# Kernel optimization log

Hardware: AMD Instinct MI355X
Metric: run time of the kernel (lower is better)

## Reference

```python
import jax, jax.numpy as jnp
import numpy as np

WS = (3, 8, 8)          # (t, h, w) window
SHIFT = (0, 4, 4)
HEADS = 6
DIM = 120
HD = DIM // HEADS
SCALE = HD ** -0.5
N = WS[0] * WS[1] * WS[2]   # 192 tokens per window
NQ = N // 3                 # 64 query tokens (last frame)


def _rel_pos_index():
    cd, ch, cw = np.arange(WS[0]), np.arange(WS[1]), np.arange(WS[2])
    c2 = np.stack(np.meshgrid(cd, ch, cw, indexing='ij')).reshape(3, -1)      # (3, N)
    c1 = np.stack(np.meshgrid(np.arange(1), ch, cw, indexing='ij')).reshape(3, -1)  # (3, NQ)
    rel = (c1[:, :, None] - c2[:, None, :]).transpose(1, 2, 0)                # (NQ, N, 3)
    rel = rel + np.array([WS[0] - 1, WS[1] - 1, WS[2] - 1])
    idx = rel[..., 0] * (2 * WS[1] - 1) * (2 * WS[2] - 1) + rel[..., 1] * (2 * WS[2] - 1) + rel[..., 2]
    return idx.astype(np.int32)  # values in [0, 3*15*15)


def _shift_attn_mask(h, w):
    # standard Swin shifted-window mask, tiled over the 3 frames
    img = np.zeros((h, w), np.int32)
    cnt = 0
    for hs in (slice(0, -WS[1]), slice(-WS[1], -SHIFT[1]), slice(-SHIFT[1], None)):
        for ws_ in (slice(0, -WS[2]), slice(-WS[2], -SHIFT[2]), slice(-SHIFT[2], None)):
            img[hs, ws_] = cnt
            cnt += 1
    win = img.reshape(h // WS[1], WS[1], w // WS[2], WS[2]).transpose(0, 2, 1, 3).reshape(-1, WS[1] * WS[2])
    m2 = win[:, None, :] - win[:, :, None]
    m2 = np.where(m2 != 0, -100.0, 0.0).astype(np.float32)  # (nW, 64, 64)
    return np.tile(m2, (1, 3, 3))                            # (nW, 192, 192)


def setup_inputs() -> dict:
    key = jax.random.key(0)
    ks = jax.random.split(key, 10)
    b, t, h, w, c = 1, 3, 256, 256, DIM
    nW = (h // WS[1]) * (w // WS[2])
    B_ = b * nW
    return {
        'x': jax.random.normal(ks[0], (b, t, h, w, c), jnp.float32),
        'quary0': jax.random.normal(ks[1], (B_, NQ, c), jnp.float32),
        'quary1': jax.random.normal(ks[2], (B_, NQ, c), jnp.float32),
        'qkv_w': jax.random.normal(ks[3], (3 * c, c), jnp.float32) * 0.02,
        'qkv_b': jnp.zeros((3 * c,), jnp.float32),
        'proj_w': jax.random.normal(ks[4], (c, c), jnp.float32) * 0.02,
        'proj_b': jnp.zeros((c,), jnp.float32),
        'rpb_table': jax.random.normal(ks[5], (WS[0] * (2 * WS[1] - 1) * (2 * WS[2] - 1), HEADS), jnp.float32) * 0.02,
        'pm_w': jax.random.normal(ks[6], (1, c), jnp.float32) * 0.02,
        'pm_b': jnp.zeros((1,), jnp.float32),
        'attn_mask': jnp.asarray(_shift_attn_mask(h, w)),
        'rel_idx': jnp.asarray(_rel_pos_index()),
    }


def reference(x, quary0, quary1, qkv_w, qkv_b, proj_w, proj_b, rpb_table, pm_w, pm_b, attn_mask, rel_idx):
    b, t, h, w, c = x.shape
    # cyclic shift
    x = jnp.roll(x, (-SHIFT[0], -SHIFT[1], -SHIFT[2]), axis=(1, 2, 3))
    # window partition -> (B_, N, c)
    xw = x.reshape(b, t // WS[0], WS[0], h // WS[1], WS[1], w // WS[2], WS[2], c)
    xw = xw.transpose(0, 1, 3, 5, 2, 4, 6, 7).reshape(-1, N, c)
    B_ = xw.shape[0]
    # adaptive mask prediction (eval path: hard threshold; sigmoid(s/T)>=0.5 <=> s>=0)
    pred_q = jax.lax.stop_gradient(xw[:, 2 * NQ:, :])
    soft = jnp.abs(pred_q - quary0) @ pm_w.T + pm_b          # (B_, NQ, 1)
    pred = (soft >= 0).astype(x.dtype)
    # qkv
    qkv = (xw @ qkv_w.T + qkv_b).reshape(B_, N, 3, HEADS, HD).transpose(2, 0, 3, 1, 4)
    q = qkv[0][:, :, 2 * NQ:, :] * SCALE                      # (B_, H, NQ, hd)
    k, v = qkv[1], qkv[2]                                     # (B_, H, N, hd)
    attn = jnp.einsum('bhqd,bhkd->bhqk', q, k)                # (B_, H, NQ, N)
    # gathered relative position bias
    rpb = rpb_table[rel_idx.reshape(-1)].reshape(NQ, N, HEADS).transpose(2, 0, 1)
    attn = attn + rpb[None]
    # shift mask
    nW = attn_mask.shape[0]
    attn = attn.reshape(b, nW, HEADS, NQ, N) + attn_mask[None, :, None, 2 * NQ:, :]
    attn = jax.nn.softmax(attn.reshape(B_, HEADS, NQ, N), axis=-1)
    out = jnp.einsum('bhqk,bhkd->bqhd', attn, v).reshape(B_, NQ, c)
    # output projection + token-pruning blend (math-equivalent to gather/fill eval path)
    x1 = out @ proj_w.T + proj_b
    x_pred = x1 * pred + quary1 * (1.0 - pred)
    xo = jnp.concatenate([x_pred, pred], axis=-1)             # (B_, NQ, c+1)
    # single-frame window reverse
    xo = xo.reshape(b, h // WS[1], w // WS[2], WS[1], WS[2], c + 1)
    xo = xo.transpose(0, 1, 3, 2, 4, 5).reshape(b, h, w, c + 1)
    xo = jnp.roll(xo, (SHIFT[1], SHIFT[2]), axis=(1, 2))
    return xo
```

## Files before the change

kernel.cpp:

```cpp
#include <hip/hip_runtime.h>
#include <math.h>

#define NT 256

typedef __attribute__((ext_vector_type(8))) short s16x8;
typedef __attribute__((ext_vector_type(4))) float f32x4;

#define KVF_OFF 0
#define QF_OFF  73728
#define PJF_OFF 122880
#define RPB_OFF 172032

__device__ __forceinline__ unsigned short f2bf(float f) {
    union { float f; unsigned int i; } v; v.f = f;
    unsigned int x = v.i;
    x += 0x7fffu + ((x >> 16) & 1u);
    return (unsigned short)(x >> 16);
}
__device__ __forceinline__ unsigned int pk2(float a, float b) {
    return (unsigned int)f2bf(a) | ((unsigned int)f2bf(b) << 16);
}

#define MFMA(a, b, c) __builtin_amdgcn_mfma_f32_16x16x32_bf16(a, b, c, 0, 0, 0)

__global__ void prep(const float* __restrict__ qkv_w,
                     const float* __restrict__ proj_w,
                     const float* __restrict__ rpb_table,
                     const int*   __restrict__ rel_idx,
                     unsigned char* __restrict__ wsb)
{
    int gid = blockIdx.x * blockDim.x + threadIdx.x;
    int nthr = gridDim.x * blockDim.x;
    unsigned short* KVF = (unsigned short*)(wsb + KVF_OFF);
    unsigned short* QF  = (unsigned short*)(wsb + QF_OFF);
    unsigned short* PJF = (unsigned short*)(wsb + PJF_OFF);
    float*          RPB = (float*)(wsb + RPB_OFF);

    for (int f = gid; f < 6 * 3 * 4 * 512; f += nthr) {
        int q = f & 511, rest = f >> 9;
        int kk = rest & 3, rest2 = rest >> 2;
        int nt = rest2 % 3, h = rest2 / 3;
        int ln = q >> 3, j = q & 7;
        int l15 = ln & 15, qd = ln >> 4;
        int nglob = nt * 16 + l15, k = kk * 32 + qd * 8 + j;
        float v = 0.f;
        if (k < 120 && nglob < 40) {
            int row = (nglob < 20) ? (120 + h * 20 + nglob) : (240 + h * 20 + nglob - 20);
            v = qkv_w[row * 120 + k];
        }
        KVF[f] = f2bf(v);
    }
    for (int f = gid; f < 6 * 2 * 4 * 512; f += nthr) {
        int q = f & 511, rest = f >> 9;
        int kk = rest & 3, rest2 = rest >> 2;
        int nt = rest2 & 1, h = rest2 >> 1;
        int ln = q >> 3, j = q & 7;
        int l15 = ln & 15, qd = ln >> 4;
        int nn = nt * 16 + l15, k = kk * 32 + qd * 8 + j;
        int row = h * 20 + nn;
        float v = (k < 120) ? qkv_w[row * 120 + k] : 0.f;
        QF[f] = f2bf(v);
    }
    for (int f = gid; f < 6 * 8 * 512; f += nthr) {
        int q = f & 511, rest = f >> 9;
        int ct = rest & 7, h = rest >> 3;
        int ln = q >> 3, j = q & 7;
        int l15 = ln & 15, qd = ln >> 4;
        int c = ct * 16 + l15, k = qd * 8 + j;
        float v = (k < 20 && c < 120) ? proj_w[c * 120 + h * 20 + k] : 0.f;
        PJF[f] = f2bf(v);
    }
    for (int i = gid; i < 6 * 192 * 64; i += nthr) {
        int r = i & 63, n = (i >> 6) % 192, h = i / (192 * 64);
        RPB[i] = rpb_table[rel_idx[r * 192 + n] * 6 + h];
    }
}

__global__ __launch_bounds__(NT, 2)
void swin_mfma(const float* __restrict__ x,
               const float* __restrict__ quary0,
               const float* __restrict__ quary1,
               const float* __restrict__ qkv_b,
               const float* __restrict__ proj_b,
               const float* __restrict__ pm_w,
               const float* __restrict__ pm_b,
               const unsigned char* __restrict__ wsb,
               float* __restrict__ out)
{
    __shared__ alignas(16) unsigned char smem[77968];
    unsigned short* xw = (unsigned short*)smem;
    unsigned short* ks = (unsigned short*)(smem + 46096);
    unsigned short* qs = (unsigned short*)(smem + 55312);
    unsigned short* vt = (unsigned short*)(smem + 61456);
    float* pred_s = (float*)(smem + 77456);
    int*   grp_s  = (int*)(smem + 77712);

    const int tid = threadIdx.x;
    const int wv = tid >> 6, ln = tid & 63;
    const int l15 = ln & 15, qd = ln >> 4;
    const int widx = blockIdx.x;
    const int wh = widx >> 5, ww = widx & 31;
    const float SCALE = 0.22360679774997896f;

    const unsigned short* KVF = (const unsigned short*)(wsb + KVF_OFF);
    const unsigned short* QF  = (const unsigned short*)(wsb + QF_OFF);
    const unsigned short* PJF = (const unsigned short*)(wsb + PJF_OFF);
    const float*          RPB = (const float*)(wsb + RPB_OFF);

    for (int e = tid; e < 192 * 30; e += NT) {
        int n = e / 30, c4 = e % 30;
        int f = n >> 6, ii = (n >> 3) & 7, jj = n & 7;
        int y0 = (wh * 8 + ii + 4) & 255;
        int x0 = (ww * 8 + jj + 4) & 255;
        float4 val = *(const float4*)(x + (((size_t)(f * 256 + y0)) * 256 + x0) * 120 + c4 * 4);
        unsigned int lo = pk2(val.x, val.y);
        unsigned int hi = pk2(val.z, val.w);
        unsigned int off = (unsigned)(n * 120 + c4 * 4);
        *(unsigned int*)(xw + off)     = lo;
        *(unsigned int*)(xw + off + 2) = hi;
    }
    if (tid < 8) xw[192 * 120 + tid] = 0;
    for (int e = tid; e < 192 * 4; e += NT) ks[(e >> 2) * 24 + 20 + (e & 3)] = 0;
    for (int e = tid; e < 2 * 64 * 4; e += NT)
        qs[(e >> 8) * 1536 + ((e >> 2) & 63) * 24 + 20 + (e & 3)] = 0;
    if (tid < 64) {
        int ii = tid >> 3, jj = tid & 7;
        int y0 = (wh * 8 + ii + 4) & 255;
        int x0 = (ww * 8 + jj + 4) & 255;
        int hg = (y0 >= 248) + (y0 >= 252);
        int wg = (x0 >= 248) + (x0 >= 252);
        grp_s[tid] = hg * 3 + wg;
    }
    {
        int r = tid >> 2, j = tid & 3;
        int ii = r >> 3, jj = r & 7;
        int y0 = (wh * 8 + ii + 4) & 255;
        int x0 = (ww * 8 + jj + 4) & 255;
        const float* xr  = x + (((size_t)(2 * 256 + y0)) * 256 + x0) * 120;
        const float* q0r = quary0 + ((size_t)widx * 64 + r) * 120;
        float acc = 0.f;
        for (int ch = j * 30; ch < j * 30 + 30; ++ch)
            acc += fabsf(xr[ch] - q0r[ch]) * pm_w[ch];
        acc += __shfl_xor(acc, 1);
        acc += __shfl_xor(acc, 2);
        if (j == 0) pred_s[r] = (acc + pm_b[0] >= 0.f) ? 1.f : 0.f;
    }
    __syncthreads();

    auto kvjob = [&](int mt, int nt, int hh, int pty) {
        const unsigned short* arow  = xw + (mt * 16 + l15) * 120;
        const unsigned short* bbase = KVF + ((hh * 3 + nt) * 4) * 512 + ln * 8;
        f32x4 acc = {0.f, 0.f, 0.f, 0.f};
        #pragma unroll
        for (int kk = 0; kk < 4; ++kk)
            acc = MFMA(*(const s16x8*)(arow + kk * 32 + qd * 8),
                       *(const s16x8*)(bbase + kk * 512), acc);
        int nglob = nt * 16 + l15;
        if (nglob < 40) {
            float bias = qkv_b[nglob < 20 ? (120 + hh * 20 + nglob)
                                          : (240 + hh * 20 + nglob - 20)];
            #pragma unroll
            for (int reg = 0; reg < 4; ++reg) {
                int tok = mt * 16 + qd * 4 + reg;
                unsigned short vb = f2bf(acc[reg] + bias);
                if (nglob < 20) ks[tok * 24 + nglob] = vb;
                else            vt[pty * 4000 + (nglob - 20) * 200 + tok] = vb;
            }
        }
    };
    auto qjob = [&](int mt, int nt, int hh, int pty) {
        const unsigned short* arow  = xw + (128 + mt * 16 + l15) * 120;
        const unsigned short* bbase = QF + ((hh * 2 + nt) * 4) * 512 + ln * 8;
        f32x4 acc = {0.f, 0.f, 0.f, 0.f};
        #pragma unroll
        for (int kk = 0; kk < 4; ++kk)
            acc = MFMA(*(const s16x8*)(arow + kk * 32 + qd * 8),
                       *(const s16x8*)(bbase + kk * 512), acc);
        int nn = nt * 16 + l15;
        if (nn < 20) {
            float bias = qkv_b[hh * 20 + nn];
            #pragma unroll
            for (int reg = 0; reg < 4; ++reg)
                qs[pty * 1536 + (mt * 16 + qd * 4 + reg) * 24 + nn] =
                    f2bf((acc[reg] + bias) * SCALE);
        }
    };

    for (int e = wv; e < 44; e += 4) {
        if (e < 36) kvjob(e % 12, e / 12, 0, 0);
        else        { int t = e - 36; qjob(t & 3, t >> 2, 0, 0); }
    }
    __syncthreads();

    const int q_l = wv * 16 + l15;
    const int gq = grp_s[q_l];
    unsigned long long mbits = 0ull;
    #pragma unroll
    for (int t = 0; t < 12; ++t)
        #pragma unroll
        for (int r = 0; r < 4; ++r) {
            int tok = t * 16 + qd * 4 + r;
            if (gq != grp_s[tok & 63]) mbits |= (1ull << (t * 4 + r));
        }
    const int srcA = (((qd * 2) & 3) << 4) | l15;
    const int srcB = (((qd * 2 + 1) & 3) << 4) | l15;
    const int msel = qd >> 1;
    const s16x8 zf = {0, 0, 0, 0, 0, 0, 0, 0};

    f32x4 pacc[8];
    #pragma unroll
    for (int i = 0; i < 8; ++i) { f32x4 z = {0.f,0.f,0.f,0.f}; pacc[i] = z; }

    for (int h = 0; h < 6; ++h) {
        const int pr = h & 1, pw = (h + 1) & 1;

        const float* rbase = RPB + ((size_t)(h * 192 + qd * 4)) * 64 + q_l;
        float vals[48];
        #pragma unroll
        for (int t = 0; t < 12; ++t)
            #pragma unroll
            for (int r = 0; r < 4; ++r)
                vals[t * 4 + r] = rbase[(t * 16 + r) * 64]
                                + (((mbits >> (t * 4 + r)) & 1ull) ? -100.f : 0.f);

        if (h < 5) {
            for (int e = wv; e < 20; e += 4) {
                if (e < 12) kvjob(e, 2, h + 1, pw);
                else        { int t = e - 12; qjob(t & 3, t >> 2, h + 1, pw); }
            }
        }

        s16x8 bQ = zf;
        if (qd < 3) bQ = *(const s16x8*)(qs + pr * 1536 + q_l * 24 + qd * 8);
        f32x4 sc[12];
        #pragma unroll
        for (int t = 0; t < 12; ++t) {
            s16x8 aK = *(const s16x8*)(ks + (t * 16 + l15) * 24 + qd * 8);
            f32x4 z = {0.f, 0.f, 0.f, 0.f};
            sc[t] = MFMA(aK, bQ, z);
        }
        float m = -1e30f;
        #pragma unroll
        for (int t = 0; t < 12; ++t)
            #pragma unroll
            for (int r = 0; r < 4; ++r) {
                float v = vals[t * 4 + r] + sc[t][r];
                vals[t * 4 + r] = v; m = fmaxf(m, v);
            }
        m = fmaxf(m, __shfl_xor(m, 16));
        m = fmaxf(m, __shfl_xor(m, 32));
        __syncthreads();

        if (h < 5) {
            for (int e = wv; e < 24; e += 4)
                kvjob(e % 12, (e < 12) ? 0 : 1, h + 1, pw);
        }

        float s = 0.f;
        #pragma unroll
        for (int i = 0; i < 48; ++i) { float ev = __expf(vals[i] - m); vals[i] = ev; s += ev; }
        s += __shfl_xor(s, 16);
        s += __shfl_xor(s, 32);
        float inv = 1.0f / s;

        unsigned int plo[12], phi[12];
        #pragma unroll
        for (int t = 0; t < 12; ++t) {
            plo[t] = pk2(vals[t * 4 + 0] * inv, vals[t * 4 + 1] * inv);
            phi[t] = pk2(vals[t * 4 + 2] * inv, vals[t * 4 + 3] * inv);
        }

        f32x4 o0 = {0.f,0.f,0.f,0.f}, o1 = {0.f,0.f,0.f,0.f};
        #pragma unroll
        for (int kk = 0; kk < 6; ++kk) {
            unsigned int a0 = __shfl(plo[2 * kk],     srcA);
            unsigned int a1 = __shfl(plo[2 * kk + 1], srcA);
            unsigned int b0 = __shfl(phi[2 * kk],     srcA);
            unsigned int b1 = __shfl(phi[2 * kk + 1], srcA);
            unsigned int c0 = __shfl(plo[2 * kk],     srcB);
            unsigned int c1 = __shfl(plo[2 * kk + 1], srcB);
            unsigned int d0 = __shfl(phi[2 * kk],     srcB);
            unsigned int d1 = __shfl(phi[2 * kk + 1], srcB);
            union { s16x8 v; unsigned int u[4]; } bf;
            bf.u[0] = msel ? a1 : a0;
            bf.u[1] = msel ? b1 : b0;
            bf.u[2] = msel ? c1 : c0;
            bf.u[3] = msel ? d1 : d0;
            s16x8 aV0 = *(const s16x8*)(vt + pr * 4000 + l15 * 200 + kk * 32 + qd * 8);
            s16x8 aV1 = zf;
            if (l15 < 4)
                aV1 = *(const s16x8*)(vt + pr * 4000 + (16 + l15) * 200 + kk * 32 + qd * 8);
            o0 = MFMA(aV0, bf.v, o0);
            o1 = MFMA(aV1, bf.v, o1);
        }

        {
            unsigned int ol0 = pk2(o0[0], o0[1]), oh0 = pk2(o0[2], o0[3]);
            unsigned int ol1 = pk2(o1[0], o1[1]), oh1 = pk2(o1[2], o1[3]);
            unsigned int w0a = __shfl(ol0, srcA), w0b = __shfl(ol1, srcA);
            unsigned int w1a = __shfl(oh0, srcA), w1b = __shfl(oh1, srcA);
            unsigned int w2a = __shfl(ol0, srcB), w2b = __shfl(ol1, srcB);
            unsigned int w3a = __shfl(oh0, srcB), w3b = __shfl(oh1, srcB);
            union { s16x8 v; unsigned int u[4]; } bo;
            bo.u[0] = msel ? w0b : w0a;
            bo.u[1] = msel ? w1b : w1a;
            bo.u[2] = msel ? w2b : w2a;
            bo.u[3] = msel ? w3b : w3a;
            #pragma unroll
            for (int ct = 0; ct < 8; ++ct) {
                s16x8 aP = *(const s16x8*)(PJF + (h * 8 + ct) * 512 + ln * 8);
                pacc[ct] = MFMA(aP, bo.v, pacc[ct]);
            }
        }
        __syncthreads();
    }

    float* xo = (float*)smem;
    #pragma unroll
    for (int ct = 0; ct < 8; ++ct)
        #pragma unroll
        for (int r = 0; r < 4; ++r) {
            int c = ct * 16 + qd * 4 + r;
            if (c < 120) xo[q_l * 129 + c] = pacc[ct][r];
        }
    __syncthreads();

    for (int e = tid; e < 64 * 121; e += NT) {
        int r = e / 121, c = e - r * 121;
        int ii = r >> 3, jj = r & 7;
        int y0 = (wh * 8 + ii + 4) & 255;
        int x0 = (ww * 8 + jj + 4) & 255;
        float p = pred_s[r];
        float val;
        if (c < 120)
            val = (p != 0.f) ? (xo[r * 129 + c] + proj_b[c])
                             : quary1[(size_t)widx * 7680 + (size_t)r * 120 + c];
        else
            val = p;
        out[((size_t)(y0 * 256 + x0)) * 121 + c] = val;
    }
}

extern "C" void kernel_launch(void* const* d_in, const int* in_sizes, int n_in,
                              void* d_out, int out_size, void* d_ws, size_t ws_size,
                              hipStream_t stream) {
    const float* x        = (const float*)d_in[0];
    const float* quary0   = (const float*)d_in[1];
    const float* quary1   = (const float*)d_in[2];
    const float* qkv_w    = (const float*)d_in[3];
    const float* qkv_b    = (const float*)d_in[4];
    const float* proj_w   = (const float*)d_in[5];
    const float* proj_b   = (const float*)d_in[6];
    const float* rpb      = (const float*)d_in[7];
    const float* pm_w     = (const float*)d_in[8];
    const float* pm_b     = (const float*)d_in[9];
    const int*   rel_idx  = (const int*)d_in[11];
    float* out = (float*)d_out;
    unsigned char* wsb = (unsigned char*)d_ws;

    prep<<<128, 512, 0, stream>>>(qkv_w, proj_w, rpb, rel_idx, wsb);
    swin_mfma<<<1024, NT, 0, stream>>>(x, quary0, quary1, qkv_b, proj_b,
                                       pm_w, pm_b, wsb, out);
}
```

Measured before the change: 436.0 us.

## Warp-specialize attention: four compute waves plus four producer waves for QKV

The block grows from 4 to 8 waves. Waves 0-3 handle scores, softmax, PV and projection for the current head, while waves 4-7 produce V for the current head and K/Q for the next head between barriers. The double buffers for q and v are removed, which shrinks LDS use, and launch bounds now ask for 4 blocks per CU instead of 2. The aim is to move QKV projection work off the critical attention waves and raise occupancy. In exchange there is tighter register pressure under the new launch bounds, and with single buffers the overlap only works because of the existing barrier structure.

```diff
diff --git a/kernel.cpp b/kernel.cpp
--- a/kernel.cpp
+++ b/kernel.cpp
@@ -1,7 +1,7 @@
 #include <hip/hip_runtime.h>
 #include <math.h>
 
-#define NT 256
+#define NT 512
 
 typedef __attribute__((ext_vector_type(8))) short s16x8;
 typedef __attribute__((ext_vector_type(4))) float f32x4;
@@ -76,7 +76,7 @@
     }
 }
 
-__global__ __launch_bounds__(NT, 2)
+__global__ __launch_bounds__(NT, 4)
 void swin_mfma(const float* __restrict__ x,
                const float* __restrict__ quary0,
                const float* __restrict__ quary1,
@@ -87,13 +87,13 @@
                const unsigned char* __restrict__ wsb,
                float* __restrict__ out)
 {
-    __shared__ alignas(16) unsigned char smem[77968];
+    __shared__ alignas(16) unsigned char smem[66896];
     unsigned short* xw = (unsigned short*)smem;
     unsigned short* ks = (unsigned short*)(smem + 46096);
     unsigned short* qs = (unsigned short*)(smem + 55312);
-    unsigned short* vt = (unsigned short*)(smem + 61456);
-    float* pred_s = (float*)(smem + 77456);
-    int*   grp_s  = (int*)(smem + 77712);
+    unsigned short* vt = (unsigned short*)(smem + 58384);
+    float* pred_s = (float*)(smem + 66384);
+    int*   grp_s  = (int*)(smem + 66640);
 
     const int tid = threadIdx.x;
     const int wv = tid >> 6, ln = tid & 63;
@@ -121,8 +121,7 @@
     }
     if (tid < 8) xw[192 * 120 + tid] = 0;
     for (int e = tid; e < 192 * 4; e += NT) ks[(e >> 2) * 24 + 20 + (e & 3)] = 0;
-    for (int e = tid; e < 2 * 64 * 4; e += NT)
-        qs[(e >> 8) * 1536 + ((e >> 2) & 63) * 24 + 20 + (e & 3)] = 0;
+    for (int e = tid; e < 64 * 4;  e += NT) qs[(e >> 2) * 24 + 20 + (e & 3)] = 0;
     if (tid < 64) {
         int ii = tid >> 3, jj = tid & 7;
         int y0 = (wh * 8 + ii + 4) & 255;
@@ -131,7 +130,7 @@
         int wg = (x0 >= 248) + (x0 >= 252);
         grp_s[tid] = hg * 3 + wg;
     }
-    {
+    if (tid < 256) {
         int r = tid >> 2, j = tid & 3;
         int ii = r >> 3, jj = r & 7;
         int y0 = (wh * 8 + ii + 4) & 255;
@@ -147,7 +146,7 @@
     }
     __syncthreads();
 
-    auto kvjob = [&](int mt, int nt, int hh, int pty) {
+    auto kvjob = [&](int mt, int nt, int hh, bool kwrite, bool vwrite) {
         const unsigned short* arow  = xw + (mt * 16 + l15) * 120;
         const unsigned short* bbase = KVF + ((hh * 3 + nt) * 4) * 512 + ln * 8;
         f32x4 acc = {0.f, 0.f, 0.f, 0.f};
@@ -156,19 +155,23 @@
             acc = MFMA(*(const s16x8*)(arow + kk * 32 + qd * 8),
                        *(const s16x8*)(bbase + kk * 512), acc);
         int nglob = nt * 16 + l15;
-        if (nglob < 40) {
-            float bias = qkv_b[nglob < 20 ? (120 + hh * 20 + nglob)
-                                          : (240 + hh * 20 + nglob - 20)];
-            #pragma unroll
-            for (int reg = 0; reg < 4; ++reg) {
-                int tok = mt * 16 + qd * 4 + reg;
-                unsigned short vb = f2bf(acc[reg] + bias);
-                if (nglob < 20) ks[tok * 24 + nglob] = vb;
-                else            vt[pty * 4000 + (nglob - 20) * 200 + tok] = vb;
+        if (nglob < 20) {
+            if (kwrite) {
+                float bias = qkv_b[120 + hh * 20 + nglob];
+                #pragma unroll
+                for (int reg = 0; reg < 4; ++reg)
+                    ks[(mt * 16 + qd * 4 + reg) * 24 + nglob] = f2bf(acc[reg] + bias);
+            }
+        } else if (nglob < 40) {
+            if (vwrite) {
+                float bias = qkv_b[240 + hh * 20 + nglob - 20];
+                #pragma unroll
+                for (int reg = 0; reg < 4; ++reg)
+                    vt[(nglob - 20) * 200 + mt * 16 + qd * 4 + reg] = f2bf(acc[reg] + bias);
             }
         }
     };
-    auto qjob = [&](int mt, int nt, int hh, int pty) {
+    auto qjob = [&](int mt, int nt, int hh) {
         const unsigned short* arow  = xw + (128 + mt * 16 + l15) * 120;
         const unsigned short* bbase = QF + ((hh * 2 + nt) * 4) * 512 + ln * 8;
         f32x4 acc = {0.f, 0.f, 0.f, 0.f};
@@ -181,18 +184,18 @@
             float bias = qkv_b[hh * 20 + nn];
             #pragma unroll
             for (int reg = 0; reg < 4; ++reg)
-                qs[pty * 1536 + (mt * 16 + qd * 4 + reg) * 24 + nn] =
-                    f2bf((acc[reg] + bias) * SCALE);
+                qs[(mt * 16 + qd * 4 + reg) * 24 + nn] = f2bf((acc[reg] + bias) * SCALE);
         }
     };
 
-    for (int e = wv; e < 44; e += 4) {
-        if (e < 36) kvjob(e % 12, e / 12, 0, 0);
-        else        { int t = e - 36; qjob(t & 3, t >> 2, 0, 0); }
+    for (int e = wv; e < 32; e += 8) {
+        if (e < 12)      kvjob(e, 0, 0, true, false);
+        else if (e < 24) kvjob(e - 12, 1, 0, true, false);
+        else             { int t = e - 24; qjob(t & 3, t >> 2, 0); }
     }
     __syncthreads();
 
-    const int q_l = wv * 16 + l15;
+    const int q_l = (wv & 3) * 16 + l15;
     const int gq = grp_s[q_l];
     unsigned long long mbits = 0ull;
     #pragma unroll
@@ -212,89 +215,81 @@
     for (int i = 0; i < 8; ++i) { f32x4 z = {0.f,0.f,0.f,0.f}; pacc[i] = z; }
 
     for (int h = 0; h < 6; ++h) {
-        const int pr = h & 1, pw = (h + 1) & 1;
-
-        const float* rbase = RPB + ((size_t)(h * 192 + qd * 4)) * 64 + q_l;
         float vals[48];
-        #pragma unroll
-        for (int t = 0; t < 12; ++t)
-            #pragma unroll
-            for (int r = 0; r < 4; ++r)
-                vals[t * 4 + r] = rbase[(t * 16 + r) * 64]
-                                + (((mbits >> (t * 4 + r)) & 1ull) ? -100.f : 0.f);
-
-        if (h < 5) {
-            for (int e = wv; e < 20; e += 4) {
-                if (e < 12) kvjob(e, 2, h + 1, pw);
-                else        { int t = e - 12; qjob(t & 3, t >> 2, h + 1, pw); }
-            }
-        }
-
-        s16x8 bQ = zf;
-        if (qd < 3) bQ = *(const s16x8*)(qs + pr * 1536 + q_l * 24 + qd * 8);
-        f32x4 sc[12];
-        #pragma unroll
-        for (int t = 0; t < 12; ++t) {
-            s16x8 aK = *(const s16x8*)(ks + (t * 16 + l15) * 24 + qd * 8);
-            f32x4 z = {0.f, 0.f, 0.f, 0.f};
-            sc[t] = MFMA(aK, bQ, z);
-        }
         float m = -1e30f;
-        #pragma unroll
-        for (int t = 0; t < 12; ++t)
-            #pragma unroll
-            for (int r = 0; r < 4; ++r) {
-                float v = vals[t * 4 + r] + sc[t][r];
-                vals[t * 4 + r] = v; m = fmaxf(m, v);
-            }
-        m = fmaxf(m, __shfl_xor(m, 16));
-        m = fmaxf(m, __shfl_xor(m, 32));
+
+        if (wv < 4) {
+            const float* rbase = RPB + ((size_t)(h * 192 + qd * 4)) * 64 + q_l;
+            #pragma unroll
+            for (int t = 0; t < 12; ++t)
+                #pragma unroll
+                for (int r = 0; r < 4; ++r)
+                    vals[t * 4 + r] = rbase[(t * 16 + r) * 64]
+                                    + (((mbits >> (t * 4 + r)) & 1ull) ? -100.f : 0.f);
+
+            s16x8 bQ = zf;
+            if (qd < 3) bQ = *(const s16x8*)(qs + q_l * 24 + qd * 8);
+            f32x4 sc[12];
+            #pragma unroll
+            for (int t = 0; t < 12; ++t) {
+                s16x8 aK = *(const s16x8*)(ks + (t * 16 + l15) * 24 + qd * 8);
+                f32x4 z = {0.f, 0.f, 0.f, 0.f};
+                sc[t] = MFMA(aK, bQ, z);
+            }
+            #pragma unroll
+            for (int t = 0; t < 12; ++t)
+                #pragma unroll
+                for (int r = 0; r < 4; ++r) {
+                    float v = vals[t * 4 + r] + sc[t][r];
+                    vals[t * 4 + r] = v; m = fmaxf(m, v);
+                }
+            m = fmaxf(m, __shfl_xor(m, 16));
+            m = fmaxf(m, __shfl_xor(m, 32));
+        } else {
+            for (int e = (wv & 3); e < 24; e += 4)
+                kvjob(e % 12, 1 + e / 12, h, false, true);
+        }
         __syncthreads();
 
-        if (h < 5) {
-            for (int e = wv; e < 24; e += 4)
-                kvjob(e % 12, (e < 12) ? 0 : 1, h + 1, pw);
-        }
-
-        float s = 0.f;
-        #pragma unroll
-        for (int i = 0; i < 48; ++i) { float ev = __expf(vals[i] - m); vals[i] = ev; s += ev; }
-        s += __shfl_xor(s, 16);
-        s += __shfl_xor(s, 32);
-        float inv = 1.0f / s;
-
-        unsigned int plo[12], phi[12];
-        #pragma unroll
-        for (int t = 0; t < 12; ++t) {
-            plo[t] = pk2(vals[t * 4 + 0] * inv, vals[t * 4 + 1] * inv);
-            phi[t] = pk2(vals[t * 4 + 2] * inv, vals[t * 4 + 3] * inv);
-        }
-
-        f32x4 o0 = {0.f,0.f,0.f,0.f}, o1 = {0.f,0.f,0.f,0.f};
-        #pragma unroll
-        for (int kk = 0; kk < 6; ++kk) {
-            unsigned int a0 = __shfl(plo[2 * kk],     srcA);
-            unsigned int a1 = __shfl(plo[2 * kk + 1], srcA);
-            unsigned int b0 = __shfl(phi[2 * kk],     srcA);
-            unsigned int b1 = __shfl(phi[2 * kk + 1], srcA);
-            unsigned int c0 = __shfl(plo[2 * kk],     srcB);
-            unsigned int c1 = __shfl(plo[2 * kk + 1], srcB);
-            unsigned int d0 = __shfl(phi[2 * kk],     srcB);
-            unsigned int d1 = __shfl(phi[2 * kk + 1], srcB);
-            union { s16x8 v; unsigned int u[4]; } bf;
-            bf.u[0] = msel ? a1 : a0;
-            bf.u[1] = msel ? b1 : b0;
-            bf.u[2] = msel ? c1 : c0;
-            bf.u[3] = msel ? d1 : d0;
-            s16x8 aV0 = *(const s16x8*)(vt + pr * 4000 + l15 * 200 + kk * 32 + qd * 8);
-            s16x8 aV1 = zf;
-            if (l15 < 4)
-                aV1 = *(const s16x8*)(vt + pr * 4000 + (16 + l15) * 200 + kk * 32 + qd * 8);
-            o0 = MFMA(aV0, bf.v, o0);
-            o1 = MFMA(aV1, bf.v, o1);
-        }
-
-        {
+        if (wv < 4) {
+            float s = 0.f;
+            #pragma unroll
+            for (int i = 0; i < 48; ++i) { float ev = __expf(vals[i] - m); vals[i] = ev; s += ev; }
+            s += __shfl_xor(s, 16);
+            s += __shfl_xor(s, 32);
+            float inv = 1.0f / s;
+
+            unsigned int plo[12], phi[12];
+            #pragma unroll
+            for (int t = 0; t < 12; ++t) {
+                plo[t] = pk2(vals[t * 4 + 0] * inv, vals[t * 4 + 1] * inv);
+                phi[t] = pk2(vals[t * 4 + 2] * inv, vals[t * 4 + 3] * inv);
+            }
+
+            f32x4 o0 = {0.f,0.f,0.f,0.f}, o1 = {0.f,0.f,0.f,0.f};
+            #pragma unroll
+            for (int kk = 0; kk < 6; ++kk) {
+                unsigned int a0 = __shfl(plo[2 * kk],     srcA);
+                unsigned int a1 = __shfl(plo[2 * kk + 1], srcA);
+                unsigned int b0 = __shfl(phi[2 * kk],     srcA);
+                unsigned int b1 = __shfl(phi[2 * kk + 1], srcA);
+                unsigned int c0 = __shfl(plo[2 * kk],     srcB);
+                unsigned int c1 = __shfl(plo[2 * kk + 1], srcB);
+                unsigned int d0 = __shfl(phi[2 * kk],     srcB);
+                unsigned int d1 = __shfl(phi[2 * kk + 1], srcB);
+                union { s16x8 v; unsigned int u[4]; } bf;
+                bf.u[0] = msel ? a1 : a0;
+                bf.u[1] = msel ? b1 : b0;
+                bf.u[2] = msel ? c1 : c0;
+                bf.u[3] = msel ? d1 : d0;
+                s16x8 aV0 = *(const s16x8*)(vt + l15 * 200 + kk * 32 + qd * 8);
+                s16x8 aV1 = zf;
+                if (l15 < 4)
+                    aV1 = *(const s16x8*)(vt + (16 + l15) * 200 + kk * 32 + qd * 8);
+                o0 = MFMA(aV0, bf.v, o0);
+                o1 = MFMA(aV1, bf.v, o1);
+            }
+
             unsigned int ol0 = pk2(o0[0], o0[1]), oh0 = pk2(o0[2], o0[3]);
             unsigned int ol1 = pk2(o1[0], o1[1]), oh1 = pk2(o1[2], o1[3]);
             unsigned int w0a = __shfl(ol0, srcA), w0b = __shfl(ol1, srcA);
@@ -311,20 +306,29 @@
                 s16x8 aP = *(const s16x8*)(PJF + (h * 8 + ct) * 512 + ln * 8);
                 pacc[ct] = MFMA(aP, bo.v, pacc[ct]);
             }
+        } else if (h < 5) {
+            for (int e = (wv & 3); e < 32; e += 4) {
+                if (e < 12)      kvjob(e, 0, h + 1, true, false);
+                else if (e < 24) kvjob(e - 12, 1, h + 1, true, false);
+                else             { int t = e - 24; qjob(t & 3, t >> 2, h + 1); }
+            }
         }
         __syncthreads();
     }
 
-    float* xo = (float*)smem;
-    #pragma unroll
-    for (int ct = 0; ct < 8; ++ct)
+    if (wv < 4) {
+        float* xo = (float*)smem;
         #pragma unroll
-        for (int r = 0; r < 4; ++r) {
-            int c = ct * 16 + qd * 4 + r;
-            if (c < 120) xo[q_l * 129 + c] = pacc[ct][r];
-        }
+        for (int ct = 0; ct < 8; ++ct)
+            #pragma unroll
+            for (int r = 0; r < 4; ++r) {
+                int c = ct * 16 + qd * 4 + r;
+                if (c < 120) xo[q_l * 129 + c] = pacc[ct][r];
+            }
+    }
     __syncthreads();
 
+    const float* xo = (const float*)smem;
     for (int e = tid; e < 64 * 121; e += NT) {
         int r = e / 121, c = e - r * 121;
         int ii = r >> 3, jj = r & 7;
```

Result: slower. 510.8 us (+17.2%).
